# Kernel optimization log

Hardware: AMD Instinct MI355X
Metric: run time of the kernel (lower is better)

## Reference

```python
import jax, jax.numpy as jnp
import numpy as np

BLOCK_SIZE = 128


def setup_inputs() -> dict:
    key = jax.random.key(0)
    kq, kk, kv = jax.random.split(key, 3)
    B, H, S, D = 2, 16, 4096, 64
    q = jax.random.normal(kq, (B, H, S, D), dtype=jnp.float32)
    k = jax.random.normal(kk, (B, H, S, D), dtype=jnp.float32)
    v = jax.random.normal(kv, (B, H, S, D), dtype=jnp.float32)
    return {"q": q, "k": k, "v": v}


def _flash_attn(q, k, v, block_size=BLOCK_SIZE):
    # Faithful translation of FlashAttentionImpl (use_fp8=False, causal=False,
    # mask=None, deterministic=True), including its exact online recurrence
    # (which uses exp(scores - block_max) rather than exp(scores - new_max)).
    B, H, Sq, D = q.shape
    Sk = k.shape[2]
    nb = Sk // block_size  # Sk divisible by block_size by construction
    scale = 1.0 / jnp.sqrt(jnp.asarray(D, q.dtype))

    # [nb, B, H, block, D] for scanning over K/V blocks
    kb = k.reshape(B, H, nb, block_size, D).transpose(2, 0, 1, 3, 4)
    vb = v.reshape(B, H, nb, block_size, D).transpose(2, 0, 1, 3, 4)

    o0 = jnp.zeros((B, H, Sq, D), dtype=q.dtype)
    n0 = jnp.zeros((B, H, Sq, 1), dtype=q.dtype)
    m0 = jnp.full((B, H, Sq, 1), -jnp.inf, dtype=q.dtype)

    def step(carry, blk):
        o_acc, norm_acc, m_acc = carry
        k_blk, v_blk = blk  # [B,H,block,D]
        scores = jnp.einsum('bhqd,bhkd->bhqk', q, k_blk,
                            precision=jax.lax.Precision.HIGHEST) * scale
        block_max = jnp.max(scores, axis=-1, keepdims=True)
        new_max = jnp.maximum(m_acc, block_max)
        exp_scale = jnp.exp(m_acc - new_max)
        exp_scores = jnp.exp(scores - block_max)
        norm_new = norm_acc * exp_scale + jnp.sum(exp_scores, axis=-1, keepdims=True)
        o_new = o_acc * exp_scale + jnp.einsum(
            'bhqk,bhkd->bhqd', exp_scores, v_blk,
            precision=jax.lax.Precision.HIGHEST)
        return (o_new, norm_new, new_max), None

    (o, norm, _), _ = jax.lax.scan(step, (o0, n0, m0), (kb, vb))
    return o / (norm + 1e-06)


def reference(q, k, v):
    return _flash_attn(q, k, v)
```

## Files before the change

kernel.cpp:

```cpp
#include <hip/hip_runtime.h>
#include <cstdint>
#include <cstddef>

typedef float     f32x16 __attribute__((ext_vector_type(16)));
typedef _Float16  f16x8  __attribute__((ext_vector_type(8)));
typedef __bf16    bf16x8 __attribute__((ext_vector_type(8)));
typedef unsigned  u32x2  __attribute__((ext_vector_type(2)));
typedef unsigned  u32x4  __attribute__((ext_vector_type(4)));

static_assert(sizeof(f16x8) == 16, "f16x8 must be 16B");

#define DEV __device__ __forceinline__

DEV unsigned short f2h_bits(float f) {
    _Float16 h = (_Float16)f;
    return __builtin_bit_cast(unsigned short, h);
}
DEV unsigned pack2h(float a, float b) {
    return (unsigned)f2h_bits(a) | ((unsigned)f2h_bits(b) << 16);
}

DEV unsigned f2bf_bits(float f) {
    unsigned u = __builtin_bit_cast(unsigned, f);
    return ((u + 0x7fffu + ((u >> 16) & 1u)) >> 16) & 0xffffu;
}
DEV float bf2f(unsigned bits) {
    return __builtin_bit_cast(float, bits << 16);
}
DEV unsigned pack2(float a, float b) {
    return f2bf_bits(a) | (f2bf_bits(b) << 16);
}

typedef __attribute__((address_space(1))) const void gas_t;
typedef __attribute__((address_space(3))) void       las_t;
DEV void gload_lds16(const void* g, void* l) {
    __builtin_amdgcn_global_load_lds((gas_t*)g, (las_t*)l, 16, 0, 0);
}

constexpr int D     = 64;
constexpr int SLEN  = 4096;
constexpr int KBLK  = 128;
constexpr int NBLK  = SLEN / KBLK;
constexpr int QTILE = 128;
constexpr int VSTR  = 136;
constexpr int NBH   = 32;
constexpr size_t IMG = 8192;
constexpr size_t TEN = (size_t)NBH * NBLK * IMG;

__global__ __launch_bounds__(256, 2)
void prep16(const float* __restrict__ Kg, const float* __restrict__ Vg,
            unsigned short* __restrict__ kf_g, unsigned short* __restrict__ vt_g)
{
    __shared__ __align__(16) unsigned short vstage[IMG];

    const int tid = threadIdx.x;
    const int kb  = blockIdx.x;
    const int bh  = blockIdx.y;
    const long base = (long)bh * SLEN * D;
    const int  kv0  = kb * KBLK;
    const size_t img = (size_t)(bh * NBLK + kb) * IMG;

#pragma unroll
    for (int i = 0; i < 4; ++i) {
        int chunk = i * 256 + tid;
        int ki  = chunk >> 8;
        int c   = (chunk >> 6) & 3;
        int cl  = chunk & 63;
        int row = ki * 32 + (cl & 31);
        int d0  = c * 16 + (cl >> 5) * 8;
        const float* kp = Kg + base + (long)(kv0 + row) * D + d0;
        float4 x0 = *(const float4*)kp;
        float4 x1 = *(const float4*)(kp + 4);
        u32x4 H;
        H.x = pack2h(x0.x, x0.y);
        H.y = pack2h(x0.z, x0.w);
        H.z = pack2h(x1.x, x1.y);
        H.w = pack2h(x1.z, x1.w);
        *(u32x4*)&kf_g[img + (size_t)chunk * 8] = H;
    }

    const int e  = tid & 3;
    const int e0 = e & 1, e1 = e >> 1;
    const int DQi = (tid >> 2) & 15;
    const int w   = tid >> 6;
#pragma unroll
    for (int i = 0; i < 8; ++i) {
        int KQ = (i * 4 + w) * 4;
        int DQ = DQi * 4;
        float4 x = *(const float4*)(Vg + base + (long)(kv0 + KQ + e) * D + DQ);
        float f0 = x.x, f1 = x.y, f2 = x.z, f3 = x.w;
        float sA0 = e0 ? f0 : f1, sA1 = e0 ? f2 : f3;
        float rA0 = __shfl_xor(sA0, 1, 64), rA1 = __shfl_xor(sA1, 1, 64);
        float A0 = e0 ? rA0 : f0, A1 = e0 ? f1 : rA0;
        float A2 = e0 ? rA1 : f2, A3 = e0 ? f3 : rA1;
        float sB0 = e1 ? A0 : A2, sB1 = e1 ? A1 : A3;
        float rB0 = __shfl_xor(sB0, 2, 64), rB1 = __shfl_xor(sB1, 2, 64);
        float B0 = e1 ? rB0 : A0, B1 = e1 ? rB1 : A1;
        float B2 = e1 ? A2 : rB0, B3 = e1 ? A3 : rB1;
        int d = DQ + e;
        u32x2 p;
        p.x = pack2h(B0, B1);
        p.y = pack2h(B2, B3);
        int off = d * 128 + (KQ ^ ((d & 7) << 3));
        *(u32x2*)&vstage[off] = p;
    }

    __syncthreads();

#pragma unroll
    for (int i = 0; i < 4; ++i) {
        size_t t8 = (size_t)(i * 256 + tid) * 8;
        *(u32x4*)&vt_g[img + t8] = *(const u32x4*)&vstage[t8];
    }
}

__global__ __launch_bounds__(256, 3)
void fa_fwd3(const float* __restrict__ Qg,
             const unsigned short* __restrict__ kf_g,
             const unsigned short* __restrict__ vt_g,
             float* __restrict__ Og)
{
    __shared__ __align__(16) unsigned short kf_l[IMG];
    __shared__ __align__(16) unsigned short vt_l[IMG];

    const int tid = threadIdx.x;
    const int l   = tid & 63;
    const int w   = tid >> 6;
    const int h   = l >> 5;
    const int ln  = l & 31;

    const int  bh   = blockIdx.y;
    const long base = (long)bh * SLEN * D;
    const float* Qb = Qg + base;
    float*       Ob = Og + base;

    const int qrow = blockIdx.x * QTILE + w * 32 + ln;
    f16x8 qf[4];
#pragma unroll
    for (int c = 0; c < 4; ++c) {
        const float* qp = Qb + (long)qrow * D + c * 16 + h * 8;
        float4 x0 = *(const float4*)qp;
        float4 x1 = *(const float4*)(qp + 4);
        u32x4 H;
        H.x = pack2h(x0.x * 0.125f, x0.y * 0.125f);
        H.y = pack2h(x0.z * 0.125f, x0.w * 0.125f);
        H.z = pack2h(x1.x * 0.125f, x1.y * 0.125f);
        H.w = pack2h(x1.z * 0.125f, x1.w * 0.125f);
        qf[c] = __builtin_bit_cast(f16x8, H);
    }

    f32x16 oa0 = {};
    f32x16 oa1 = {};
    f32x16 st[4];

    float mrun = -INFINITY;
    float norm = 0.0f;

#pragma unroll 1
    for (int kb = 0; kb < NBLK; ++kb) {
        const size_t img = (size_t)(bh * NBLK + kb) * IMG;
        const unsigned short* kfs = kf_g + img;
        const unsigned short* vts = vt_g + img;

#pragma unroll
        for (int i = 0; i < 4; ++i) {
            int o = (i * 256 + w * 64) * 8;
            int g = o + l * 8;
            gload_lds16(kfs + g, &kf_l[o]);
            gload_lds16(vts + g, &vt_l[o]);
        }

        __syncthreads();

#pragma unroll
        for (int ki = 0; ki < 4; ++ki) {
            f32x16 acc = {};
#pragma unroll
            for (int c = 0; c < 4; ++c) {
                int ch = (ki * 4 + c) * 64 + l;
                f16x8 a = *(const f16x8*)&kf_l[ch * 8];
                acc = __builtin_amdgcn_mfma_f32_32x32x16_f16(a, qf[c], acc, 0, 0, 0);
            }
            st[ki] = acc;
        }

        float bm = -INFINITY;
#pragma unroll
        for (int ki = 0; ki < 4; ++ki)
#pragma unroll
            for (int r = 0; r < 16; ++r) bm = fmaxf(bm, st[ki][r]);
        bm = fmaxf(bm, __shfl_xor(bm, 32, 64));

        float newm = fmaxf(mrun, bm);
        float sc   = __expf(mrun - newm);
        mrun = newm;

        float psum = 0.0f;
#pragma unroll
        for (int ki = 0; ki < 4; ++ki) {
#pragma unroll
            for (int r = 0; r < 16; ++r) {
                float p = __expf(st[ki][r] - bm);
                st[ki][r] = p;
                psum += p;
            }
        }
        psum += __shfl_xor(psum, 32, 64);
        norm = norm * sc + psum;

        if (__any(sc != 1.0f)) {
#pragma unroll
            for (int r = 0; r < 16; ++r) { oa0[r] *= sc; oa1[r] *= sc; }
        }

        f16x8 pf[8];
#pragma unroll
        for (int c = 0; c < 8; ++c) {
            int ki = c >> 1, half = c & 1;
            int rb = half * 8;
            unsigned A0 = pack2h(st[ki][rb + 0], st[ki][rb + 1]);
            unsigned A1 = pack2h(st[ki][rb + 2], st[ki][rb + 3]);
            unsigned B0 = pack2h(st[ki][rb + 4], st[ki][rb + 5]);
            unsigned B1 = pack2h(st[ki][rb + 6], st[ki][rb + 7]);
            unsigned s0 = h ? A0 : B0;
            unsigned s1 = h ? A1 : B1;
            unsigned r0 = (unsigned)__shfl_xor((int)s0, 32, 64);
            unsigned r1 = (unsigned)__shfl_xor((int)s1, 32, 64);
            u32x4 f;
            f.x = h ? r0 : A0;
            f.y = h ? r1 : A1;
            f.z = h ? B0 : r0;
            f.w = h ? B1 : r1;
            pf[c] = __builtin_bit_cast(f16x8, f);
        }

#pragma unroll
        for (int c = 0; c < 8; ++c) {
            const int kvo = c * 16 + h * 8;
            const int sa  = ln * 128 + (kvo ^ ((ln & 7) << 3));
            f16x8 va = *(const f16x8*)&vt_l[sa];
            f16x8 vb = *(const f16x8*)&vt_l[sa + 4096];
            oa0 = __builtin_amdgcn_mfma_f32_32x32x16_f16(va, pf[c], oa0, 0, 0, 0);
            oa1 = __builtin_amdgcn_mfma_f32_32x32x16_f16(vb, pf[c], oa1, 0, 0, 0);
        }

        __syncthreads();
    }

    float inv = 1.0f / (norm + 1e-6f);
    long  orow = (long)qrow * D;
#pragma unroll
    for (int rg = 0; rg < 4; ++rg) {
        int d0 = 8 * rg + 4 * h;
        float4 w0, w1;
        w0.x = oa0[4 * rg + 0] * inv;
        w0.y = oa0[4 * rg + 1] * inv;
        w0.z = oa0[4 * rg + 2] * inv;
        w0.w = oa0[4 * rg + 3] * inv;
        w1.x = oa1[4 * rg + 0] * inv;
        w1.y = oa1[4 * rg + 1] * inv;
        w1.z = oa1[4 * rg + 2] * inv;
        w1.w = oa1[4 * rg + 3] * inv;
        *(float4*)(Ob + orow + d0)      = w0;
        *(float4*)(Ob + orow + 32 + d0) = w1;
    }
}

__global__ __launch_bounds__(256, 2)
void fa_fwd(const float* __restrict__ Qg, const float* __restrict__ Kg,
            const float* __restrict__ Vg, float* __restrict__ Og)
{
    __shared__ __align__(16) unsigned short khi[KBLK * D];
    __shared__ __align__(16) unsigned short klo[KBLK * D];
    __shared__ __align__(16) unsigned short vt[D * VSTR];

    const int tid = threadIdx.x;
    const int l   = tid & 63;
    const int w   = tid >> 6;
    const int h   = l >> 5;
    const int ln  = l & 31;

    const int  bh   = blockIdx.y;
    const long base = (long)bh * SLEN * D;
    const float* Qb = Qg + base;
    const float* Kb = Kg + base;
    const float* Vb = Vg + base;
    float*       Ob = Og + base;

    const int qrow = blockIdx.x * QTILE + w * 32 + ln;
    bf16x8 qhi[4], qlo[4];
#pragma unroll
    for (int c = 0; c < 4; ++c) {
        const float* qp = Qb + (long)qrow * D + c * 16 + h * 8;
        float4 x0 = *(const float4*)qp;
        float4 x1 = *(const float4*)(qp + 4);
        float xs[8] = {x0.x, x0.y, x0.z, x0.w, x1.x, x1.y, x1.z, x1.w};
        unsigned hw[4], lw[4];
#pragma unroll
        for (int j = 0; j < 4; ++j) {
            float a = xs[2 * j] * 0.125f, b = xs[2 * j + 1] * 0.125f;
            unsigned ha = f2bf_bits(a), hb = f2bf_bits(b);
            lw[j] = f2bf_bits(a - bf2f(ha)) | (f2bf_bits(b - bf2f(hb)) << 16);
            hw[j] = ha | (hb << 16);
        }
        u32x4 H = {hw[0], hw[1], hw[2], hw[3]};
        u32x4 L = {lw[0], lw[1], lw[2], lw[3]};
        qhi[c] = __builtin_bit_cast(bf16x8, H);
        qlo[c] = __builtin_bit_cast(bf16x8, L);
    }

    f32x16 oa0 = {};
    f32x16 oa1 = {};
    f32x16 st[4];

    float mrun = -INFINITY;
    float norm = 0.0f;

    const int e  = tid & 3;
    const int e0 = e & 1, e1 = e >> 1;
    const int DQi = (tid >> 2) & 15;

#pragma unroll 1
    for (int kb = 0; kb < NBLK; ++kb) {
        const int kv0 = kb * KBLK;

#pragma unroll
        for (int i = 0; i < 4; ++i) {
            int chunk = i * 256 + tid;
            int ki  = chunk >> 8;
            int c   = (chunk >> 6) & 3;
            int cl  = chunk & 63;
            int row = ki * 32 + (cl & 31);
            int d0  = c * 16 + (cl >> 5) * 8;
            const float* kp = Kb + (long)(kv0 + row) * D + d0;
            float4 x0 = *(const float4*)kp;
            float4 x1 = *(const float4*)(kp + 4);
            float xs[8] = {x0.x, x0.y, x0.z, x0.w, x1.x, x1.y, x1.z, x1.w};
            unsigned hw[4], lw[4];
#pragma unroll
            for (int j = 0; j < 4; ++j) {
                float a = xs[2 * j], b = xs[2 * j + 1];
                unsigned ha = f2bf_bits(a), hb = f2bf_bits(b);
                lw[j] = f2bf_bits(a - bf2f(ha)) | (f2bf_bits(b - bf2f(hb)) << 16);
                hw[j] = ha | (hb << 16);
            }
            u32x4 H = {hw[0], hw[1], hw[2], hw[3]};
            u32x4 L = {lw[0], lw[1], lw[2], lw[3]};
            *(u32x4*)&khi[chunk * 8] = H;
            *(u32x4*)&klo[chunk * 8] = L;
        }

#pragma unroll
        for (int i = 0; i < 8; ++i) {
            int KQ = (i * 4 + w) * 4;
            int DQ = DQi * 4;
            float4 x = *(const float4*)(Vb + (long)(kv0 + KQ + e) * D + DQ);
            float f0 = x.x, f1 = x.y, f2 = x.z, f3 = x.w;
            float sA0 = e0 ? f0 : f1, sA1 = e0 ? f2 : f3;
            float rA0 = __shfl_xor(sA0, 1, 64), rA1 = __shfl_xor(sA1, 1, 64);
            float A0 = e0 ? rA0 : f0, A1 = e0 ? f1 : rA0;
            float A2 = e0 ? rA1 : f2, A3 = e0 ? f3 : rA1;
            float sB0 = e1 ? A0 : A2, sB1 = e1 ? A1 : A3;
            float rB0 = __shfl_xor(sB0, 2, 64), rB1 = __shfl_xor(sB1, 2, 64);
            float B0 = e1 ? rB0 : A0, B1 = e1 ? rB1 : A1;
            float B2 = e1 ? A2 : rB0, B3 = e1 ? A3 : rB1;
            u32x2 p;
            p.x = pack2(B0, B1);
            p.y = pack2(B2, B3);
            *(u32x2*)&vt[(DQ + e) * VSTR + KQ] = p;
        }

        __syncthreads();

#pragma unroll
        for (int ki = 0; ki < 4; ++ki) {
            f32x16 acc = {};
#pragma unroll
            for (int c = 0; c < 4; ++c) {
                int ch = (ki * 4 + c) * 64 + l;
                bf16x8 ah = *(const bf16x8*)&khi[ch * 8];
                bf16x8 al = *(const bf16x8*)&klo[ch * 8];
                acc = __builtin_amdgcn_mfma_f32_32x32x16_bf16(ah, qhi[c], acc, 0, 0, 0);
                acc = __builtin_amdgcn_mfma_f32_32x32x16_bf16(ah, qlo[c], acc, 0, 0, 0);
                acc = __builtin_amdgcn_mfma_f32_32x32x16_bf16(al, qhi[c], acc, 0, 0, 0);
            }
            st[ki] = acc;
        }

        float bm = -INFINITY;
#pragma unroll
        for (int ki = 0; ki < 4; ++ki)
#pragma unroll
            for (int r = 0; r < 16; ++r) bm = fmaxf(bm, st[ki][r]);
        bm = fmaxf(bm, __shfl_xor(bm, 32, 64));

        float newm = fmaxf(mrun, bm);
        float sc   = __expf(mrun - newm);
        mrun = newm;

        float psum = 0.0f;
#pragma unroll
        for (int ki = 0; ki < 4; ++ki) {
#pragma unroll
            for (int r = 0; r < 16; ++r) {
                float p = __expf(st[ki][r] - bm);
                st[ki][r] = p;
                psum += p;
            }
        }
        psum += __shfl_xor(psum, 32, 64);
        norm = norm * sc + psum;

#pragma unroll
        for (int r = 0; r < 16; ++r) { oa0[r] *= sc; oa1[r] *= sc; }

        bf16x8 pf[8];
#pragma unroll
        for (int c = 0; c < 8; ++c) {
            int ki = c >> 1, half = c & 1;
            int rb = half * 8;
            unsigned A0 = pack2(st[ki][rb + 0], st[ki][rb + 1]);
            unsigned A1 = pack2(st[ki][rb + 2], st[ki][rb + 3]);
            unsigned B0 = pack2(st[ki][rb + 4], st[ki][rb + 5]);
            unsigned B1 = pack2(st[ki][rb + 6], st[ki][rb + 7]);
            unsigned s0 = h ? A0 : B0;
            unsigned s1 = h ? A1 : B1;
            unsigned r0 = (unsigned)__shfl_xor((int)s0, 32, 64);
            unsigned r1 = (unsigned)__shfl_xor((int)s1, 32, 64);
            u32x4 f;
            f.x = h ? r0 : A0;
            f.y = h ? r1 : A1;
            f.z = h ? B0 : r0;
            f.w = h ? B1 : r1;
            pf[c] = __builtin_bit_cast(bf16x8, f);
        }

#pragma unroll
        for (int c = 0; c < 8; ++c) {
            const int kvo = c * 16 + h * 8;
            bf16x8 va = *(const bf16x8*)&vt[(ln)      * VSTR + kvo];
            bf16x8 vb = *(const bf16x8*)&vt[(32 + ln) * VSTR + kvo];
            oa0 = __builtin_amdgcn_mfma_f32_32x32x16_bf16(va, pf[c], oa0, 0, 0, 0);
            oa1 = __builtin_amdgcn_mfma_f32_32x32x16_bf16(vb, pf[c], oa1, 0, 0, 0);
        }

        __syncthreads();
    }

    float inv = 1.0f / (norm + 1e-6f);
    long  orow = (long)qrow * D;
#pragma unroll
    for (int rg = 0; rg < 4; ++rg) {
        int d0 = 8 * rg + 4 * h;
        float4 w0, w1;
        w0.x = oa0[4 * rg + 0] * inv;
        w0.y = oa0[4 * rg + 1] * inv;
        w0.z = oa0[4 * rg + 2] * inv;
        w0.w = oa0[4 * rg + 3] * inv;
        w1.x = oa1[4 * rg + 0] * inv;
        w1.y = oa1[4 * rg + 1] * inv;
        w1.z = oa1[4 * rg + 2] * inv;
        w1.w = oa1[4 * rg + 3] * inv;
        *(float4*)(Ob + orow + d0)      = w0;
        *(float4*)(Ob + orow + 32 + d0) = w1;
    }
}

extern "C" void kernel_launch(void* const* d_in, const int* in_sizes, int n_in,
                              void* d_out, int out_size, void* d_ws, size_t ws_size,
                              hipStream_t stream)
{
    (void)in_sizes; (void)n_in; (void)out_size;
    const float* q = (const float*)d_in[0];
    const float* k = (const float*)d_in[1];
    const float* v = (const float*)d_in[2];
    float*       o = (float*)d_out;

    const size_t need = 2 * TEN * sizeof(unsigned short);

    if (ws_size >= need) {
        unsigned short* kf_g = (unsigned short*)d_ws;
        unsigned short* vt_g = kf_g + TEN;

        dim3 pgrid(NBLK, NBH);
        hipLaunchKernelGGL(prep16, pgrid, dim3(256), 0, stream, k, v, kf_g, vt_g);

        dim3 grid(SLEN / QTILE, NBH);
        hipLaunchKernelGGL(fa_fwd3, grid, dim3(256), 0, stream, q, kf_g, vt_g, o);
    } else {
        dim3 grid(SLEN / QTILE, NBH);
        hipLaunchKernelGGL(fa_fwd, grid, dim3(256), 0, stream, q, k, v, o);
    }
}
```

Before: 340.3 us.

## Double-buffer K/V tiles in LDS and use exp2 with hardware conversion

The attention kernel now keeps two LDS buffers for K/V and prefetches the next block with async global-to-LDS loads while computing on the current one. This hides load latency behind the MFMA and softmax work. Softmax uses v_exp_f32 (exp2) with log2(e) folded into the Q scale, and probabilities are packed with v_cvt_pkrtz. The prep kernel stages K through LDS so its global reads and writes are coalesced. The cost is twice the LDS per block, with launch bounds lowered from 3 to 2 blocks per CU, and round-toward-zero fp16 packing of P.

New measurement: 308.4 us. 1.1x faster.

```diff
diff --git a/kernel.cpp b/kernel.cpp
--- a/kernel.cpp
+++ b/kernel.cpp
@@ -18,6 +18,16 @@
 }
 DEV unsigned pack2h(float a, float b) {
     return (unsigned)f2h_bits(a) | ((unsigned)f2h_bits(b) << 16);
+}
+DEV unsigned cvt_pkrtz(float a, float b) {
+    unsigned r;
+    asm("v_cvt_pkrtz_f16_f32 %0, %1, %2" : "=v"(r) : "v"(a), "v"(b));
+    return r;
+}
+DEV float exp2_hw(float x) {
+    float r;
+    asm("v_exp_f32 %0, %1" : "=v"(r) : "v"(x));
+    return r;
 }
 
 DEV unsigned f2bf_bits(float f) {
@@ -46,11 +56,13 @@
 constexpr int NBH   = 32;
 constexpr size_t IMG = 8192;
 constexpr size_t TEN = (size_t)NBH * NBLK * IMG;
+constexpr float QSCALE = 0.125f * 1.4426950408889634f;
 
 __global__ __launch_bounds__(256, 2)
 void prep16(const float* __restrict__ Kg, const float* __restrict__ Vg,
             unsigned short* __restrict__ kf_g, unsigned short* __restrict__ vt_g)
 {
+    __shared__ __align__(16) unsigned short kstage[IMG];
     __shared__ __align__(16) unsigned short vstage[IMG];
 
     const int tid = threadIdx.x;
@@ -61,22 +73,16 @@
     const size_t img = (size_t)(bh * NBLK + kb) * IMG;
 
 #pragma unroll
-    for (int i = 0; i < 4; ++i) {
-        int chunk = i * 256 + tid;
-        int ki  = chunk >> 8;
-        int c   = (chunk >> 6) & 3;
-        int cl  = chunk & 63;
-        int row = ki * 32 + (cl & 31);
-        int d0  = c * 16 + (cl >> 5) * 8;
-        const float* kp = Kg + base + (long)(kv0 + row) * D + d0;
-        float4 x0 = *(const float4*)kp;
-        float4 x1 = *(const float4*)(kp + 4);
-        u32x4 H;
-        H.x = pack2h(x0.x, x0.y);
-        H.y = pack2h(x0.z, x0.w);
-        H.z = pack2h(x1.x, x1.y);
-        H.w = pack2h(x1.z, x1.w);
-        *(u32x4*)&kf_g[img + (size_t)chunk * 8] = H;
+    for (int i = 0; i < 8; ++i) {
+        int idx = i * 256 + tid;
+        int row = idx >> 4;
+        int dq  = idx & 15;
+        float4 x = *(const float4*)(Kg + base + (long)(kv0 + row) * D + dq * 4);
+        u32x2 p;
+        p.x = pack2h(x.x, x.y);
+        p.y = pack2h(x.z, x.w);
+        int chunk = (row >> 5) * 256 + (dq >> 2) * 64 + (((dq >> 1) & 1) * 32) + (row & 31);
+        *(u32x2*)&kstage[chunk * 8 + (dq & 1) * 4] = p;
     }
 
     const int e  = tid & 3;
@@ -110,18 +116,21 @@
 #pragma unroll
     for (int i = 0; i < 4; ++i) {
         size_t t8 = (size_t)(i * 256 + tid) * 8;
+        *(u32x4*)&kf_g[img + t8] = *(const u32x4*)&kstage[t8];
         *(u32x4*)&vt_g[img + t8] = *(const u32x4*)&vstage[t8];
     }
 }
 
-__global__ __launch_bounds__(256, 3)
-void fa_fwd3(const float* __restrict__ Qg,
+__global__ __launch_bounds__(256, 2)
+void fa_fwd4(const float* __restrict__ Qg,
              const unsigned short* __restrict__ kf_g,
              const unsigned short* __restrict__ vt_g,
              float* __restrict__ Og)
 {
-    __shared__ __align__(16) unsigned short kf_l[IMG];
-    __shared__ __align__(16) unsigned short vt_l[IMG];
+    __shared__ __align__(16) unsigned short kf_l0[IMG];
+    __shared__ __align__(16) unsigned short vt_l0[IMG];
+    __shared__ __align__(16) unsigned short kf_l1[IMG];
+    __shared__ __align__(16) unsigned short vt_l1[IMG];
 
     const int tid = threadIdx.x;
     const int l   = tid & 63;
@@ -133,6 +142,8 @@
     const long base = (long)bh * SLEN * D;
     const float* Qb = Qg + base;
     float*       Ob = Og + base;
+    const unsigned short* kf_b = kf_g + (size_t)bh * NBLK * IMG;
+    const unsigned short* vt_b = vt_g + (size_t)bh * NBLK * IMG;
 
     const int qrow = blockIdx.x * QTILE + w * 32 + ln;
     f16x8 qf[4];
@@ -142,10 +153,10 @@
         float4 x0 = *(const float4*)qp;
         float4 x1 = *(const float4*)(qp + 4);
         u32x4 H;
-        H.x = pack2h(x0.x * 0.125f, x0.y * 0.125f);
-        H.y = pack2h(x0.z * 0.125f, x0.w * 0.125f);
-        H.z = pack2h(x1.x * 0.125f, x1.y * 0.125f);
-        H.w = pack2h(x1.z * 0.125f, x1.w * 0.125f);
+        H.x = pack2h(x0.x * QSCALE, x0.y * QSCALE);
+        H.y = pack2h(x0.z * QSCALE, x0.w * QSCALE);
+        H.z = pack2h(x1.x * QSCALE, x1.y * QSCALE);
+        H.w = pack2h(x1.z * QSCALE, x1.w * QSCALE);
         qf[c] = __builtin_bit_cast(f16x8, H);
     }
 
@@ -156,96 +167,105 @@
     float mrun = -INFINITY;
     float norm = 0.0f;
 
+    const int so = (w * 64) * 8;
+    const int go = so + l * 8;
+
+    {
+        const unsigned short* kfs = kf_b;
+        const unsigned short* vts = vt_b;
+#pragma unroll
+        for (int i = 0; i < 4; ++i) {
+            gload_lds16(kfs + go + i * 2048, &kf_l0[so + i * 2048]);
+            gload_lds16(vts + go + i * 2048, &vt_l0[so + i * 2048]);
+        }
+    }
+    __syncthreads();
+
+#define FA_ITER(CURK, CURV, NXTK, NXTV, KB)                                     \
+    do {                                                                        \
+        if ((KB) + 1 < NBLK) {                                                  \
+            const unsigned short* kfs = kf_b + (size_t)((KB) + 1) * IMG;        \
+            const unsigned short* vts = vt_b + (size_t)((KB) + 1) * IMG;        \
+            _Pragma("unroll")                                                   \
+            for (int i = 0; i < 4; ++i) {                                       \
+                gload_lds16(kfs + go + i * 2048, &NXTK[so + i * 2048]);         \
+                gload_lds16(vts + go + i * 2048, &NXTV[so + i * 2048]);         \
+            }                                                                   \
+        }                                                                       \
+        _Pragma("unroll")                                                       \
+        for (int ki = 0; ki < 4; ++ki) {                                        \
+            f32x16 acc = {};                                                    \
+            _Pragma("unroll")                                                   \
+            for (int c = 0; c < 4; ++c) {                                       \
+                int ch = (ki * 4 + c) * 64 + l;                                 \
+                f16x8 a = *(const f16x8*)&CURK[ch * 8];                         \
+                acc = __builtin_amdgcn_mfma_f32_32x32x16_f16(a, qf[c], acc, 0, 0, 0); \
+            }                                                                   \
+            st[ki] = acc;                                                       \
+        }                                                                       \
+        float bm = -INFINITY;                                                   \
+        _Pragma("unroll")                                                       \
+        for (int ki = 0; ki < 4; ++ki)                                          \
+            _Pragma("unroll")                                                   \
+            for (int r = 0; r < 16; ++r) bm = fmaxf(bm, st[ki][r]);             \
+        bm = fmaxf(bm, __shfl_xor(bm, 32, 64));                                 \
+        float newm = fmaxf(mrun, bm);                                           \
+        float sc   = exp2_hw(mrun - newm);                                      \
+        mrun = newm;                                                            \
+        float psum = 0.0f;                                                      \
+        _Pragma("unroll")                                                       \
+        for (int ki = 0; ki < 4; ++ki) {                                        \
+            _Pragma("unroll")                                                   \
+            for (int r = 0; r < 16; ++r) {                                      \
+                float p = exp2_hw(st[ki][r] - bm);                              \
+                st[ki][r] = p;                                                  \
+                psum += p;                                                      \
+            }                                                                   \
+        }                                                                       \
+        psum += __shfl_xor(psum, 32, 64);                                       \
+        norm = norm * sc + psum;                                                \
+        if (__any(sc != 1.0f)) {                                                \
+            _Pragma("unroll")                                                   \
+            for (int r = 0; r < 16; ++r) { oa0[r] *= sc; oa1[r] *= sc; }        \
+        }                                                                       \
+        f16x8 pf[8];                                                            \
+        _Pragma("unroll")                                                       \
+        for (int c = 0; c < 8; ++c) {                                           \
+            int ki = c >> 1, half = c & 1;                                      \
+            int rb = half * 8;                                                  \
+            unsigned A0 = cvt_pkrtz(st[ki][rb + 0], st[ki][rb + 1]);            \
+            unsigned A1 = cvt_pkrtz(st[ki][rb + 2], st[ki][rb + 3]);            \
+            unsigned B0 = cvt_pkrtz(st[ki][rb + 4], st[ki][rb + 5]);            \
+            unsigned B1 = cvt_pkrtz(st[ki][rb + 6], st[ki][rb + 7]);            \
+            unsigned s0 = h ? A0 : B0;                                          \
+            unsigned s1 = h ? A1 : B1;                                          \
+            unsigned r0 = (unsigned)__shfl_xor((int)s0, 32, 64);                \
+            unsigned r1 = (unsigned)__shfl_xor((int)s1, 32, 64);                \
+            u32x4 f;                                                            \
+            f.x = h ? r0 : A0;                                                  \
+            f.y = h ? r1 : A1;                                                  \
+            f.z = h ? B0 : r0;                                                  \
+            f.w = h ? B1 : r1;                                                  \
+            pf[c] = __builtin_bit_cast(f16x8, f);                               \
+        }                                                                       \
+        _Pragma("unroll")                                                       \
+        for (int c = 0; c < 8; ++c) {                                           \
+            const int kvo = c * 16 + h * 8;                                     \
+            const int sa  = ln * 128 + (kvo ^ ((ln & 7) << 3));                 \
+            f16x8 va = *(const f16x8*)&CURV[sa];                                \
+            f16x8 vb = *(const f16x8*)&CURV[sa + 4096];                         \
+            oa0 = __builtin_amdgcn_mfma_f32_32x32x16_f16(va, pf[c], oa0, 0, 0, 0); \
+            oa1 = __builtin_amdgcn_mfma_f32_32x32x16_f16(vb, pf[c], oa1, 0, 0, 0); \
+        }                                                                       \
+        __syncthreads();                                                        \
+    } while (0)
+
 #pragma unroll 1
-    for (int kb = 0; kb < NBLK; ++kb) {
-        const size_t img = (size_t)(bh * NBLK + kb) * IMG;
-        const unsigned short* kfs = kf_g + img;
-        const unsigned short* vts = vt_g + img;
-
-#pragma unroll
-        for (int i = 0; i < 4; ++i) {
-            int o = (i * 256 + w * 64) * 8;
-            int g = o + l * 8;
-            gload_lds16(kfs + g, &kf_l[o]);
-            gload_lds16(vts + g, &vt_l[o]);
-        }
-
-        __syncthreads();
-
-#pragma unroll
-        for (int ki = 0; ki < 4; ++ki) {
-            f32x16 acc = {};
-#pragma unroll
-            for (int c = 0; c < 4; ++c) {
-                int ch = (ki * 4 + c) * 64 + l;
-                f16x8 a = *(const f16x8*)&kf_l[ch * 8];
-                acc = __builtin_amdgcn_mfma_f32_32x32x16_f16(a, qf[c], acc, 0, 0, 0);
-            }
-            st[ki] = acc;
-        }
-
-        float bm = -INFINITY;
-#pragma unroll
-        for (int ki = 0; ki < 4; ++ki)
-#pragma unroll
-            for (int r = 0; r < 16; ++r) bm = fmaxf(bm, st[ki][r]);
-        bm = fmaxf(bm, __shfl_xor(bm, 32, 64));
-
-        float newm = fmaxf(mrun, bm);
-        float sc   = __expf(mrun - newm);
-        mrun = newm;
-
-        float psum = 0.0f;
-#pragma unroll
-        for (int ki = 0; ki < 4; ++ki) {
-#pragma unroll
-            for (int r = 0; r < 16; ++r) {
-                float p = __expf(st[ki][r] - bm);
-                st[ki][r] = p;
-                psum += p;
-            }
-        }
-        psum += __shfl_xor(psum, 32, 64);
-        norm = norm * sc + psum;
-
-        if (__any(sc != 1.0f)) {
-#pragma unroll
-            for (int r = 0; r < 16; ++r) { oa0[r] *= sc; oa1[r] *= sc; }
-        }
-
-        f16x8 pf[8];
-#pragma unroll
-        for (int c = 0; c < 8; ++c) {
-            int ki = c >> 1, half = c & 1;
-            int rb = half * 8;
-            unsigned A0 = pack2h(st[ki][rb + 0], st[ki][rb + 1]);
-            unsigned A1 = pack2h(st[ki][rb + 2], st[ki][rb + 3]);
-            unsigned B0 = pack2h(st[ki][rb + 4], st[ki][rb + 5]);
-            unsigned B1 = pack2h(st[ki][rb + 6], st[ki][rb + 7]);
-            unsigned s0 = h ? A0 : B0;
-            unsigned s1 = h ? A1 : B1;
-            unsigned r0 = (unsigned)__shfl_xor((int)s0, 32, 64);
-            unsigned r1 = (unsigned)__shfl_xor((int)s1, 32, 64);
-            u32x4 f;
-            f.x = h ? r0 : A0;
-            f.y = h ? r1 : A1;
-            f.z = h ? B0 : r0;
-            f.w = h ? B1 : r1;
-            pf[c] = __builtin_bit_cast(f16x8, f);
-        }
-
-#pragma unroll
-        for (int c = 0; c < 8; ++c) {
-            const int kvo = c * 16 + h * 8;
-            const int sa  = ln * 128 + (kvo ^ ((ln & 7) << 3));
-            f16x8 va = *(const f16x8*)&vt_l[sa];
-            f16x8 vb = *(const f16x8*)&vt_l[sa + 4096];
-            oa0 = __builtin_amdgcn_mfma_f32_32x32x16_f16(va, pf[c], oa0, 0, 0, 0);
-            oa1 = __builtin_amdgcn_mfma_f32_32x32x16_f16(vb, pf[c], oa1, 0, 0, 0);
-        }
-
-        __syncthreads();
-    }
+    for (int kb = 0; kb < NBLK; kb += 2) {
+        FA_ITER(kf_l0, vt_l0, kf_l1, vt_l1, kb);
+        FA_ITER(kf_l1, vt_l1, kf_l0, vt_l0, kb + 1);
+    }
+#undef FA_ITER
 
     float inv = 1.0f / (norm + 1e-6f);
     long  orow = (long)qrow * D;
@@ -486,7 +506,7 @@
         hipLaunchKernelGGL(prep16, pgrid, dim3(256), 0, stream, k, v, kf_g, vt_g);
 
         dim3 grid(SLEN / QTILE, NBH);
-        hipLaunchKernelGGL(fa_fwd3, grid, dim3(256), 0, stream, q, kf_g, vt_g, o);
+        hipLaunchKernelGGL(fa_fwd4, grid, dim3(256), 0, stream, q, kf_g, vt_g, o);
     } else {
         dim3 grid(SLEN / QTILE, NBH);
         hipLaunchKernelGGL(fa_fwd, grid, dim3(256), 0, stream, q, k, v, o);
```
